# Performance work log

Hardware: AMD Instinct MI355X
Metric: run time of the kernel (lower is better)

## Reference

```python
import jax, jax.numpy as jnp
import numpy as np

N, D, DR, DA = 50000, 128, 64, 64
R, A = 2000, 5000
L, H = 2, 2
E, E2, EA = 400000, 800000, 400000


def setup_inputs() -> dict:
    key = jax.random.key(0)
    ks = jax.random.split(key, 8)
    rng = np.random.default_rng(0)

    ee = np.stack([rng.integers(0, N, E), rng.integers(0, N, E)], 1)
    ee = ee[np.lexsort((ee[:, 1], ee[:, 0]))]            # sorted unique-ish ent-ent edges
    seg_id = np.repeat(np.arange(E), 2)                  # 2 relation rows per edge
    er_rel = rng.integers(0, R, E2)
    er_index = np.stack([np.repeat(ee[:, 0], 2), er_rel], 1)   # (node, rel) pairs
    ea_index = np.stack([rng.integers(0, N, EA), rng.integers(0, A, EA)], 1)
    ea_index = ea_index[np.lexsort((ea_index[:, 1], ea_index[:, 0]))]

    s192 = 1.0 / np.sqrt(192.0)
    s320 = 1.0 / np.sqrt(320.0)
    return {
        "ent_emb": jax.random.normal(ks[0], (N, D), jnp.float32) * 0.1,
        "rel_emb": jax.random.normal(ks[1], (R, DR), jnp.float32) * 0.1,
        "attr_emb": jax.random.normal(ks[2], (A, DA), jnp.float32) * 0.1,
        "w_r": jax.random.normal(ks[3], (192, 1), jnp.float32) * s192,
        "b_r": jnp.zeros((1,), jnp.float32),
        "w_a": jax.random.normal(ks[4], (192, 1), jnp.float32) * s192,
        "b_a": jnp.zeros((1,), jnp.float32),
        "ent_attn_w": jax.random.normal(ks[5], (L, H, 192, 1), jnp.float32) * s192,
        "ent_attn_b": jnp.zeros((L, H, 1), jnp.float32),
        "con_attn_w": jax.random.normal(ks[6], (L, H, 320, 1), jnp.float32) * s320,
        "con_attn_b": jnp.zeros((L, H, 1), jnp.float32),
        "ee_index": jnp.asarray(ee, jnp.int32),
        "seg_id": jnp.asarray(seg_id, jnp.int32),
        "er_rel": jnp.asarray(er_rel, jnp.int32),
        "er_index": jnp.asarray(er_index, jnp.int32),
        "ea_index": jnp.asarray(ea_index, jnp.int32),
    }


def _leaky(v):
    return jnp.where(v > 0, v, 0.3 * v)  # LeakyReLU(alpha=0.3)


def _seg_softmax(vals, seg, n):
    m = jax.ops.segment_max(vals, seg, num_segments=n)
    e = jnp.exp(vals - m[seg])
    s = jax.ops.segment_sum(e, seg, num_segments=n)
    return e / s[seg]


def _forward(ent_emb, rel_emb, attr_emb, w_r, b_r, w_a, b_a,
             eaw, eab, caw, cab, ee_index, seg_id, er_rel, er_index, ea_index):
    n, d = ent_emb.shape
    nl, nh = eaw.shape[0], eaw.shape[1]
    dh = d // nh
    ne = ee_index.shape[0]

    def concept(idx, emb, w, b):
        feat = jnp.concatenate([ent_emb[idx[:, 0]], emb[idx[:, 1]]], axis=1)
        a = _leaky(feat @ w + b).reshape(-1)
        p = _seg_softmax(a, idx[:, 0], n)                      # tf.sparse.softmax per row
        return jax.nn.relu(jax.ops.segment_sum(p[:, None] * emb[idx[:, 1]], idx[:, 0], num_segments=n))

    concept_rel = concept(er_index, rel_emb, w_r, b_r)         # (N, DR)
    concept_attr = concept(ea_index, attr_emb, w_a, b_a)       # (N, DA)

    row, col = ee_index[:, 0], ee_index[:, 1]
    # softmax over all-ones sparse adj == neighbor mean
    deg = jax.ops.segment_sum(jnp.ones((ne,), ent_emb.dtype), row, num_segments=n)
    x = jax.ops.segment_sum(ent_emb[col], row, num_segments=n) / jnp.maximum(deg, 1.0)[:, None]

    # segment_mean of relation embeddings over duplicate (h,t) edges
    cnt = jax.ops.segment_sum(jnp.ones((er_rel.shape[0],), ent_emb.dtype), seg_id, num_segments=ne)
    rels_mean = jax.ops.segment_sum(rel_emb[er_rel], seg_id, num_segments=ne) / jnp.maximum(cnt, 1.0)[:, None]

    # concept features per edge (same for every layer/head -> hoisted)
    con_feat = jnp.concatenate([concept_rel[row], concept_attr[row], rels_mean,
                                concept_rel[col], concept_attr[col]], axis=1)  # (E, 320)

    layer_outs = []
    for l in range(nl):
        x = jax.nn.relu(x)
        heads = x.reshape(n, nh, dh)
        outs = []
        for h in range(nh):
            xe = heads[:, h, :]
            nf = xe[col]
            ef = jnp.concatenate([xe[row], rels_mean, nf], axis=1)      # (E, 192)
            ea = _leaky(ef @ eaw[l, h] + eab[l, h]).reshape(-1)
            ca = _leaky(con_feat @ caw[l, h] + cab[l, h]).reshape(-1)
            p = jax.nn.softmax(ea * ca)         # tf.nn.softmax over all edge values
            p = _seg_softmax(p, row, n)          # then tf.sparse.softmax per row
            outs.append(jax.ops.segment_sum(p[:, None] * nf, row, num_segments=n))
        x = jnp.tanh(jnp.concatenate(outs, axis=1))
        layer_outs.append(x)

    grat_out = jnp.concatenate(layer_outs, axis=1)                     # (N, L*D)
    ent_out = jnp.concatenate([grat_out, concept_rel, concept_attr], axis=1)
    conc = jnp.concatenate([concept_rel, concept_attr], axis=1)
    return ent_out, conc


def reference(ent_emb, rel_emb, attr_emb, w_r, b_r, w_a, b_a,
              ent_attn_w, ent_attn_b, con_attn_w, con_attn_b,
              ee_index, seg_id, er_rel, er_index, ea_index):
    return _forward(ent_emb, rel_emb, attr_emb, w_r, b_r, w_a, b_a,
                    ent_attn_w, ent_attn_b, con_attn_w, con_attn_b,
                    ee_index, seg_id, er_rel, er_index, ea_index)
```

## Files before the change

### kernel.cpp

```cpp
#include <hip/hip_runtime.h>
#include <math.h>

#define NENT 50000
#define RREL 2000
#define AATT 5000
#define EE   400000
#define E2   800000
#define EAE  400000
#define PB   2048

__device__ __forceinline__ float leaky(float v){ return v > 0.f ? v : 0.3f * v; }

__device__ __forceinline__ float wave_sum(float v){
#pragma unroll
  for (int m = 32; m; m >>= 1) v += __shfl_xor(v, m);
  return v;
}
__device__ __forceinline__ float sum16(float v){
#pragma unroll
  for (int m = 1; m < 16; m <<= 1) v += __shfl_xor(v, m);
  return v;
}

__device__ int lowb(const int* a, int n, int key){
  int lo = 0, hi = n;
  while (lo < hi){ int mid = (lo + hi) >> 1; if (a[2 * mid] < key) lo = mid + 1; else hi = mid; }
  return lo;
}

__global__ void k_ptr(const int* ee, const int* er, const int* ea,
                      int* pee, int* per, int* pea){
  int i = blockIdx.x * blockDim.x + threadIdx.x;
  if (i > NENT) return;
  pee[i] = lowb(ee, EE, i);
  per[i] = lowb(er, E2, i);
  pea[i] = lowb(ea, EAE, i);
}

__global__ void k_small(const float* rel_emb, const float* attr_emb,
                        const float* w_r, const float* w_a,
                        const float* eaw, const float* caw,
                        float* h_rel, float* h_attr, float4* HH0, float4* HH1){
  int t = blockIdx.x * blockDim.x + threadIdx.x;
  if (t < RREL){
    const float* e = rel_emb + (size_t)t * 64;
    float s = 0.f;
    for (int k = 0; k < 64; ++k) s += e[k] * w_r[128 + k];
    h_rel[t] = s;
    float hr[4], hc[4];
    for (int lh = 0; lh < 4; ++lh){
      float a = 0.f, c = 0.f;
      for (int k = 0; k < 64; ++k){
        a += e[k] * eaw[lh * 192 + 64 + k];
        c += e[k] * caw[lh * 320 + 128 + k];
      }
      hr[lh] = a; hc[lh] = c;
    }
    HH0[t] = make_float4(hr[0], hr[1], hc[0], hc[1]);
    HH1[t] = make_float4(hr[2], hr[3], hc[2], hc[3]);
  }
  if (t < AATT){
    const float* e = attr_emb + (size_t)t * 64;
    float s = 0.f;
    for (int k = 0; k < 64; ++k) s += e[k] * w_a[128 + k];
    h_attr[t] = s;
  }
}

__global__ void k_ent_tab(const float* ent_emb, const float* w_r, const float* w_a,
                          float* her, float* hea){
  int w = (blockIdx.x * blockDim.x + threadIdx.x) >> 6;
  int lane = threadIdx.x & 63;
  if (w >= NENT) return;
  float2 v = ((const float2*)(ent_emb + (size_t)w * 128))[lane];
  float2 a = ((const float2*)w_r)[lane];
  float2 b = ((const float2*)w_a)[lane];
  float sr = wave_sum(v.x * a.x + v.y * a.y);
  float sa = wave_sum(v.x * b.x + v.y * b.y);
  if (lane == 0){ her[w] = sr; hea[w] = sa; }
}

__global__ void k_cw(const int* er_idx, const int* ea_idx,
                     const float* her, const float* hea,
                     const float* h_rel, const float* h_attr,
                     const float* b_r, const float* b_a,
                     float* wr, float* wa){
  int e = blockIdx.x * blockDim.x + threadIdx.x;
  if (e < E2){
    int2 rc = ((const int2*)er_idx)[e];
    wr[e] = __expf(leaky(her[rc.x] + h_rel[rc.y] + b_r[0]));
  }
  if (e < EAE){
    int2 rc = ((const int2*)ea_idx)[e];
    wa[e] = __expf(leaky(hea[rc.x] + h_attr[rc.y] + b_a[0]));
  }
}

__device__ float4 concept_g(const float* wq, const int* idx, int beg, int end,
                            const float* emb, int p){
  float t = 0.f;
  for (int e = beg + p; e < end; e += 16) t += wq[e];
  t = sum16(t);
  float invz = (t > 0.f) ? (1.f / t) : 0.f;
  float4 acc = {0.f, 0.f, 0.f, 0.f};
  for (int c0 = beg; c0 < end; c0 += 8){
    int cnt = end - c0; if (cnt > 8) cnt = 8;
#pragma unroll
    for (int j = 0; j < 8; ++j){
      int e = c0 + ((j < cnt) ? j : 0);
      float wgt = wq[e] * invz;
      if (j >= cnt) wgt = 0.f;
      int obj = ((const int2*)idx)[e].y;
      float4 f = ((const float4*)(emb + (size_t)obj * 64))[p];
      acc.x = fmaf(wgt, f.x, acc.x); acc.y = fmaf(wgt, f.y, acc.y);
      acc.z = fmaf(wgt, f.z, acc.z); acc.w = fmaf(wgt, f.w, acc.w);
    }
  }
  acc.x = fmaxf(acc.x, 0.f); acc.y = fmaxf(acc.y, 0.f);
  acc.z = fmaxf(acc.z, 0.f); acc.w = fmaxf(acc.w, 0.f);
  return acc;
}

__global__ void k_phase1(const float* ent_emb, const float* rel_emb, const float* attr_emb,
                         const float* eaw, const float* caw,
                         const int* er_idx, const int* ea_idx, const int* ee,
                         const int* per, const int* pea, const int* pee,
                         const float* wr, const float* wa,
                         float4* UA0, float4* VB0, float4* UA1, float4* VB1,
                         float* out){
  int tid = blockIdx.x * blockDim.x + threadIdx.x;
  int lane = threadIdx.x & 63;
  int p = lane & 15;
  int w = (tid >> 6) * 4 + (lane >> 4);
  if (w >= NENT) return;
  float4 accR = concept_g(wr, er_idx, per[w], per[w + 1], rel_emb, p);
  float4 accA = concept_g(wa, ea_idx, pea[w], pea[w + 1], attr_emb, p);
  ((float4*)(out + (size_t)w * 384 + 256))[p] = accR;
  ((float4*)(out + (size_t)w * 384 + 320))[p] = accA;
  ((float4*)(out + (size_t)NENT * 384 + (size_t)w * 128))[p] = accR;
  ((float4*)(out + (size_t)NENT * 384 + (size_t)w * 128 + 64))[p] = accA;
  int beg = pee[w], end = pee[w + 1];
  float4 mx = {0.f,0.f,0.f,0.f}, my = {0.f,0.f,0.f,0.f};
  for (int c0 = beg; c0 < end; c0 += 4){
    int cnt = end - c0; if (cnt > 4) cnt = 4;
#pragma unroll
    for (int j = 0; j < 4; ++j){
      int e = c0 + ((j < cnt) ? j : 0);
      float msk = (j < cnt) ? 1.f : 0.f;
      int ce = ((const int2*)ee)[e].y;
      const float4* r = (const float4*)(ent_emb + (size_t)ce * 128);
      float4 q0 = r[p], q1 = r[p + 16];
      mx.x = fmaf(msk, q0.x, mx.x); mx.y = fmaf(msk, q0.y, mx.y);
      mx.z = fmaf(msk, q0.z, mx.z); mx.w = fmaf(msk, q0.w, mx.w);
      my.x = fmaf(msk, q1.x, my.x); my.y = fmaf(msk, q1.y, my.y);
      my.z = fmaf(msk, q1.z, my.z); my.w = fmaf(msk, q1.w, my.w);
    }
  }
  float invd = 1.f / fmaxf((float)(end - beg), 1.f);
  mx.x *= invd; mx.y *= invd; mx.z *= invd; mx.w *= invd;
  my.x *= invd; my.y *= invd; my.z *= invd; my.w *= invd;
  ((float4*)(out + (size_t)w * 384 + 128))[p] = mx;
  ((float4*)(out + (size_t)w * 384 + 192))[p] = my;
#pragma unroll
  for (int lh = 0; lh < 4; ++lh){
    const float* cw = caw + lh * 320;
    float4 c0 = *(const float4*)(cw + 4 * p);
    float4 c1 = *(const float4*)(cw + 64 + 4 * p);
    float4 c2 = *(const float4*)(cw + 192 + 4 * p);
    float4 c3 = *(const float4*)(cw + 256 + 4 * p);
    float av = accR.x*c0.x + accR.y*c0.y + accR.z*c0.z + accR.w*c0.w
             + accA.x*c1.x + accA.y*c1.y + accA.z*c1.z + accA.w*c1.w;
    float bv = accR.x*c2.x + accR.y*c2.y + accR.z*c2.z + accR.w*c2.w
             + accA.x*c3.x + accA.y*c3.y + accA.z*c3.z + accA.w*c3.w;
    av = sum16(av); bv = sum16(bv);
    if (p == 0){
      float4* U = (lh < 2) ? UA0 : UA1;
      float4* V = (lh < 2) ? VB0 : VB1;
      ((float*)(U + w))[2 + (lh & 1)] = av;
      ((float*)(V + w))[2 + (lh & 1)] = bv;
    }
  }
  {
    float e0 = fmaxf(mx.x,0.f), e1 = fmaxf(mx.y,0.f), e2 = fmaxf(mx.z,0.f), e3 = fmaxf(mx.w,0.f);
    float e4 = fmaxf(my.x,0.f), e5 = fmaxf(my.y,0.f), e6 = fmaxf(my.z,0.f), e7 = fmaxf(my.w,0.f);
    float4 u0 = *(const float4*)(eaw + 4 * p);
    float4 v0 = *(const float4*)(eaw + 128 + 4 * p);
    float4 u1 = *(const float4*)(eaw + 192 + 4 * p);
    float4 v1 = *(const float4*)(eaw + 192 + 128 + 4 * p);
    float pu0 = sum16(e0*u0.x + e1*u0.y + e2*u0.z + e3*u0.w);
    float pv0 = sum16(e0*v0.x + e1*v0.y + e2*v0.z + e3*v0.w);
    float pu1 = sum16(e4*u1.x + e5*u1.y + e6*u1.z + e7*u1.w);
    float pv1 = sum16(e4*v1.x + e5*v1.y + e6*v1.z + e7*v1.w);
    if (p == 0){
      ((float*)(UA0 + w))[0] = pu0; ((float*)(UA0 + w))[1] = pu1;
      ((float*)(VB0 + w))[0] = pv0; ((float*)(VB0 + w))[1] = pv1;
    }
  }
}

__global__ void k_se(const int* ee, const int* err,
                     const float4* UA, const float4* VB, const float4* HH,
                     const float* eab_l, const float* cab_l,
                     float2* s01, float* partials){
  int e = blockIdx.x * blockDim.x + threadIdx.x;
  int tid = threadIdx.x;
  __shared__ float sm0[4], sm1[4];
  float ex0 = 0.f, ex1 = 0.f;
  if (e < EE){
    int2 rc = ((const int2*)ee)[e];
    int2 rr = ((const int2*)err)[e];
    float4 ua = UA[rc.x], vb = VB[rc.y], h1 = HH[rr.x], h2 = HH[rr.y];
    float ea0 = ua.x + 0.5f * (h1.x + h2.x) + vb.x + eab_l[0];
    float ca0 = ua.z + 0.5f * (h1.z + h2.z) + vb.z + cab_l[0];
    ex0 = __expf(leaky(ea0) * leaky(ca0));
    float ea1 = ua.y + 0.5f * (h1.y + h2.y) + vb.y + eab_l[1];
    float ca1 = ua.w + 0.5f * (h1.w + h2.w) + vb.w + cab_l[1];
    ex1 = __expf(leaky(ea1) * leaky(ca1));
    s01[e] = make_float2(ex0, ex1);
  }
  float b0 = wave_sum(ex0), b1 = wave_sum(ex1);
  if ((tid & 63) == 0){ sm0[tid >> 6] = b0; sm1[tid >> 6] = b1; }
  __syncthreads();
  if (tid == 0)  partials[blockIdx.x]      = sm0[0] + sm0[1] + sm0[2] + sm0[3];
  if (tid == 64) partials[PB + blockIdx.x] = sm1[0] + sm1[1] + sm1[2] + sm1[3];
}

__global__ void k_final(const float* partials, float* scal, int nb){
  __shared__ float sm[1024];
  int tid = threadIdx.x;
  for (int h = 0; h < 2; ++h){
    float v = 0.f;
    for (int i = tid; i < nb; i += 1024) v += partials[h * PB + i];
    sm[tid] = v; __syncthreads();
    for (int s = 512; s; s >>= 1){
      if (tid < s) sm[tid] += sm[tid + s];
      __syncthreads();
    }
    if (tid == 0) scal[h] = sm[0];
    __syncthreads();
  }
}

__global__ void k_agg(const int* ee, const int* ptr, const float2* q01,
                      const float* scal, const float* xsrc, float* outp, int ocol,
                      const float* eaw_next, float4* UAn, float4* VBn){
  int tid = blockIdx.x * blockDim.x + threadIdx.x;
  int lane = threadIdx.x & 63;
  int p = lane & 15;
  int w = (tid >> 6) * 4 + (lane >> 4);
  if (w >= NENT) return;
  int beg = ptr[w], end = ptr[w + 1];
  float invZ0 = 1.f / scal[0], invZ1 = 1.f / scal[1];
  float4 a0 = {0.f,0.f,0.f,0.f}, a1 = {0.f,0.f,0.f,0.f};
  float4 b0 = {0.f,0.f,0.f,0.f}, b1 = {0.f,0.f,0.f,0.f};
  float T0 = 0.f, T1 = 0.f;
  for (int c0 = beg; c0 < end; c0 += 8){
    int cnt = end - c0; if (cnt > 8) cnt = 8;
#pragma unroll
    for (int j = 0; j < 8; ++j){
      int e = c0 + ((j < cnt) ? j : 0);
      float2 q = q01[e];
      float msk = (j < cnt) ? 1.f : 0.f;
      float s0 = q.x * msk, s1 = q.y * msk;
      T0 += s0; T1 += s1;
      int cj = ((const int2*)ee)[e].y;
      const float4* r = (const float4*)(xsrc + (size_t)cj * 384);
      float4 f0 = r[p], f1 = r[p + 16];
      f0.x = fmaxf(f0.x, 0.f); f0.y = fmaxf(f0.y, 0.f);
      f0.z = fmaxf(f0.z, 0.f); f0.w = fmaxf(f0.w, 0.f);
      f1.x = fmaxf(f1.x, 0.f); f1.y = fmaxf(f1.y, 0.f);
      f1.z = fmaxf(f1.z, 0.f); f1.w = fmaxf(f1.w, 0.f);
      b0.x = fmaf(msk, f0.x, b0.x); b0.y = fmaf(msk, f0.y, b0.y);
      b0.z = fmaf(msk, f0.z, b0.z); b0.w = fmaf(msk, f0.w, b0.w);
      b1.x = fmaf(msk, f1.x, b1.x); b1.y = fmaf(msk, f1.y, b1.y);
      b1.z = fmaf(msk, f1.z, b1.z); b1.w = fmaf(msk, f1.w, b1.w);
      a0.x = fmaf(s0, f0.x, a0.x); a0.y = fmaf(s0, f0.y, a0.y);
      a0.z = fmaf(s0, f0.z, a0.z); a0.w = fmaf(s0, f0.w, a0.w);
      a1.x = fmaf(s1, f1.x, a1.x); a1.y = fmaf(s1, f1.y, a1.y);
      a1.z = fmaf(s1, f1.z, a1.z); a1.w = fmaf(s1, f1.w, a1.w);
    }
  }
  float cnt = (float)(end - beg);
  float inv0 = (end > beg) ? (1.f / (cnt + invZ0 * T0)) : 0.f;
  float inv1 = (end > beg) ? (1.f / (cnt + invZ1 * T1)) : 0.f;
  float4 o0, o1;
  o0.x = tanhf((b0.x + invZ0 * a0.x) * inv0); o0.y = tanhf((b0.y + invZ0 * a0.y) * inv0);
  o0.z = tanhf((b0.z + invZ0 * a0.z) * inv0); o0.w = tanhf((b0.w + invZ0 * a0.w) * inv0);
  o1.x = tanhf((b1.x + invZ1 * a1.x) * inv1); o1.y = tanhf((b1.y + invZ1 * a1.y) * inv1);
  o1.z = tanhf((b1.z + invZ1 * a1.z) * inv1); o1.w = tanhf((b1.w + invZ1 * a1.w) * inv1);
  ((float4*)(outp + (size_t)w * 384 + ocol))[p]      = o0;
  ((float4*)(outp + (size_t)w * 384 + ocol + 64))[p] = o1;
  if (eaw_next){
    float e0 = fmaxf(o0.x,0.f), e1 = fmaxf(o0.y,0.f), e2 = fmaxf(o0.z,0.f), e3 = fmaxf(o0.w,0.f);
    float e4 = fmaxf(o1.x,0.f), e5 = fmaxf(o1.y,0.f), e6 = fmaxf(o1.z,0.f), e7 = fmaxf(o1.w,0.f);
    float4 u0 = *(const float4*)(eaw_next + 4 * p);
    float4 v0 = *(const float4*)(eaw_next + 128 + 4 * p);
    float4 u1 = *(const float4*)(eaw_next + 192 + 4 * p);
    float4 v1 = *(const float4*)(eaw_next + 192 + 128 + 4 * p);
    float pu0 = sum16(e0*u0.x + e1*u0.y + e2*u0.z + e3*u0.w);
    float pv0 = sum16(e0*v0.x + e1*v0.y + e2*v0.z + e3*v0.w);
    float pu1 = sum16(e4*u1.x + e5*u1.y + e6*u1.z + e7*u1.w);
    float pv1 = sum16(e4*v1.x + e5*v1.y + e6*v1.z + e7*v1.w);
    if (p == 0){
      ((float*)(UAn + w))[0] = pu0; ((float*)(UAn + w))[1] = pu1;
      ((float*)(VBn + w))[0] = pv0; ((float*)(VBn + w))[1] = pv1;
    }
  }
}

extern "C" void kernel_launch(void* const* d_in, const int* in_sizes, int n_in,
                              void* d_out, int out_size, void* d_ws, size_t ws_size,
                              hipStream_t stream){
  const float* ent_emb  = (const float*)d_in[0];
  const float* rel_emb  = (const float*)d_in[1];
  const float* attr_emb = (const float*)d_in[2];
  const float* w_r      = (const float*)d_in[3];
  const float* b_r      = (const float*)d_in[4];
  const float* w_a      = (const float*)d_in[5];
  const float* b_a      = (const float*)d_in[6];
  const float* eaw      = (const float*)d_in[7];
  const float* eab      = (const float*)d_in[8];
  const float* caw      = (const float*)d_in[9];
  const float* cab      = (const float*)d_in[10];
  const int*   ee       = (const int*)d_in[11];
  const int*   er_rel2  = (const int*)d_in[13];
  const int*   er_idx   = (const int*)d_in[14];
  const int*   ea_idx   = (const int*)d_in[15];
  float* out = (float*)d_out;

  int* pee = (int*)d_ws;
  int* per = pee + (NENT + 1);
  int* pea = per + (NENT + 1);
  float*  fbase = (float*)d_ws + 150004;
  float4* UA0 = (float4*)fbase;
  float4* VB0 = UA0 + NENT;
  float4* UA1 = VB0 + NENT;
  float4* VB1 = UA1 + NENT;
  float4* HH0 = VB1 + NENT;
  float4* HH1 = HH0 + RREL;
  float* her     = (float*)(HH1 + RREL);
  float* hea     = her + NENT;
  float* h_rel   = hea + NENT;
  float* h_attr  = h_rel + RREL;
  float* partials= h_attr + AATT;
  float* scal    = partials + 2 * PB;
  float* wr      = scal + 4;
  float* wa      = wr + E2;
  float2* s01    = (float2*)wr;

  const int nb = (EE + 255) / 256;
  const int gq = (NENT + 15) / 16;
  const int gw = (NENT + 3) / 4;

  k_ptr<<<(NENT + 1 + 255) / 256, 256, 0, stream>>>(ee, er_idx, ea_idx, pee, per, pea);
  k_small<<<(AATT + 255) / 256, 256, 0, stream>>>(rel_emb, attr_emb, w_r, w_a, eaw, caw,
                                                  h_rel, h_attr, HH0, HH1);
  k_ent_tab<<<gw, 256, 0, stream>>>(ent_emb, w_r, w_a, her, hea);
  k_cw<<<(E2 + 255) / 256, 256, 0, stream>>>(er_idx, ea_idx, her, hea,
                                             h_rel, h_attr, b_r, b_a, wr, wa);
  k_phase1<<<gq, 256, 0, stream>>>(ent_emb, rel_emb, attr_emb, eaw, caw,
                                   er_idx, ea_idx, ee, per, pea, pee, wr, wa,
                                   UA0, VB0, UA1, VB1, out);
  k_se<<<nb, 256, 0, stream>>>(ee, er_rel2, UA0, VB0, HH0, eab, cab, s01, partials);
  k_final<<<1, 1024, 0, stream>>>(partials, scal, nb);
  k_agg<<<gq, 256, 0, stream>>>(ee, pee, s01, scal, out + 128, out, 0,
                                eaw + 2 * 192, UA1, VB1);
  k_se<<<nb, 256, 0, stream>>>(ee, er_rel2, UA1, VB1, HH1, eab + 2, cab + 2, s01, partials);
  k_final<<<1, 1024, 0, stream>>>(partials, scal, nb);
  k_agg<<<gq, 256, 0, stream>>>(ee, pee, s01, scal, out, out, 128,
                                (const float*)nullptr, (float4*)nullptr, (float4*)nullptr);
}
```

Baseline: 216.5 us.

## Fuse preprocessing kernels, compute concept weights inline, fold final reduction into k_se

Merges the pointer, small-table and entity-table kernels into one block-partitioned launch. Drops the k_cw kernel and its edge-weight arrays: concept attention weights are recomputed inside phase1 and cached in shared memory for the first 64 edges per entity. The separate single-block final reduction is replaced by a last-block-done atomic counter inside k_se. Together these cut kernel launches and global traffic for the intermediate weight arrays. The cost is extra exp work in phase1, shared memory that may lower occupancy, and reliance on a threadfence/atomic pattern for correctness.

```diff
diff --git a/kernel.cpp b/kernel.cpp
--- a/kernel.cpp
+++ b/kernel.cpp
@@ -8,6 +8,8 @@
 #define E2   800000
 #define EAE  400000
 #define PB   2048
+#define PRE_PTR_B   196
+#define PRE_SMALL_B 20
 
 __device__ __forceinline__ float leaky(float v){ return v > 0.f ? v : 0.3f * v; }
 
@@ -28,89 +30,86 @@
   return lo;
 }
 
-__global__ void k_ptr(const int* ee, const int* er, const int* ea,
-                      int* pee, int* per, int* pea){
-  int i = blockIdx.x * blockDim.x + threadIdx.x;
-  if (i > NENT) return;
-  pee[i] = lowb(ee, EE, i);
-  per[i] = lowb(er, E2, i);
-  pea[i] = lowb(ea, EAE, i);
-}
-
-__global__ void k_small(const float* rel_emb, const float* attr_emb,
-                        const float* w_r, const float* w_a,
-                        const float* eaw, const float* caw,
-                        float* h_rel, float* h_attr, float4* HH0, float4* HH1){
-  int t = blockIdx.x * blockDim.x + threadIdx.x;
-  if (t < RREL){
-    const float* e = rel_emb + (size_t)t * 64;
-    float s = 0.f;
-    for (int k = 0; k < 64; ++k) s += e[k] * w_r[128 + k];
-    h_rel[t] = s;
-    float hr[4], hc[4];
-    for (int lh = 0; lh < 4; ++lh){
-      float a = 0.f, c = 0.f;
-      for (int k = 0; k < 64; ++k){
-        a += e[k] * eaw[lh * 192 + 64 + k];
-        c += e[k] * caw[lh * 320 + 128 + k];
+__global__ void k_pre(const int* ee, const int* er, const int* ea,
+                      int* pee, int* per, int* pea,
+                      const float* rel_emb, const float* attr_emb,
+                      const float* w_r, const float* w_a,
+                      const float* eaw, const float* caw,
+                      float* h_rel, float* h_attr, float4* HH0, float4* HH1,
+                      const float* ent_emb, float* her, float* hea, int* done){
+  int b = blockIdx.x;
+  if (b == 0 && threadIdx.x == 0){ done[0] = 0; done[1] = 0; }
+  if (b < PRE_PTR_B){
+    int i = b * 256 + threadIdx.x;
+    if (i <= NENT){
+      pee[i] = lowb(ee, EE, i);
+      per[i] = lowb(er, E2, i);
+      pea[i] = lowb(ea, EAE, i);
+    }
+  } else if (b < PRE_PTR_B + PRE_SMALL_B){
+    int t = (b - PRE_PTR_B) * 256 + threadIdx.x;
+    if (t < RREL){
+      const float* e = rel_emb + (size_t)t * 64;
+      float s = 0.f;
+      for (int k = 0; k < 64; ++k) s += e[k] * w_r[128 + k];
+      h_rel[t] = s;
+      float hr[4], hc[4];
+      for (int lh = 0; lh < 4; ++lh){
+        float a = 0.f, c = 0.f;
+        for (int k = 0; k < 64; ++k){
+          a += e[k] * eaw[lh * 192 + 64 + k];
+          c += e[k] * caw[lh * 320 + 128 + k];
+        }
+        hr[lh] = a; hc[lh] = c;
       }
-      hr[lh] = a; hc[lh] = c;
-    }
-    HH0[t] = make_float4(hr[0], hr[1], hc[0], hc[1]);
-    HH1[t] = make_float4(hr[2], hr[3], hc[2], hc[3]);
-  }
-  if (t < AATT){
-    const float* e = attr_emb + (size_t)t * 64;
-    float s = 0.f;
-    for (int k = 0; k < 64; ++k) s += e[k] * w_a[128 + k];
-    h_attr[t] = s;
-  }
-}
-
-__global__ void k_ent_tab(const float* ent_emb, const float* w_r, const float* w_a,
-                          float* her, float* hea){
-  int w = (blockIdx.x * blockDim.x + threadIdx.x) >> 6;
-  int lane = threadIdx.x & 63;
-  if (w >= NENT) return;
-  float2 v = ((const float2*)(ent_emb + (size_t)w * 128))[lane];
-  float2 a = ((const float2*)w_r)[lane];
-  float2 b = ((const float2*)w_a)[lane];
-  float sr = wave_sum(v.x * a.x + v.y * a.y);
-  float sa = wave_sum(v.x * b.x + v.y * b.y);
-  if (lane == 0){ her[w] = sr; hea[w] = sa; }
-}
-
-__global__ void k_cw(const int* er_idx, const int* ea_idx,
-                     const float* her, const float* hea,
-                     const float* h_rel, const float* h_attr,
-                     const float* b_r, const float* b_a,
-                     float* wr, float* wa){
-  int e = blockIdx.x * blockDim.x + threadIdx.x;
-  if (e < E2){
-    int2 rc = ((const int2*)er_idx)[e];
-    wr[e] = __expf(leaky(her[rc.x] + h_rel[rc.y] + b_r[0]));
-  }
-  if (e < EAE){
-    int2 rc = ((const int2*)ea_idx)[e];
-    wa[e] = __expf(leaky(hea[rc.x] + h_attr[rc.y] + b_a[0]));
-  }
-}
-
-__device__ float4 concept_g(const float* wq, const int* idx, int beg, int end,
-                            const float* emb, int p){
+      HH0[t] = make_float4(hr[0], hr[1], hc[0], hc[1]);
+      HH1[t] = make_float4(hr[2], hr[3], hc[2], hc[3]);
+    }
+    if (t < AATT){
+      const float* e = attr_emb + (size_t)t * 64;
+      float s = 0.f;
+      for (int k = 0; k < 64; ++k) s += e[k] * w_a[128 + k];
+      h_attr[t] = s;
+    }
+  } else {
+    int w = (((b - PRE_PTR_B - PRE_SMALL_B) * 256 + (int)threadIdx.x) >> 6);
+    int lane = threadIdx.x & 63;
+    if (w >= NENT) return;
+    float2 v = ((const float2*)(ent_emb + (size_t)w * 128))[lane];
+    float2 a = ((const float2*)w_r)[lane];
+    float2 bb = ((const float2*)w_a)[lane];
+    float sr = wave_sum(v.x * a.x + v.y * a.y);
+    float sa = wave_sum(v.x * bb.x + v.y * bb.y);
+    if (lane == 0){ her[w] = sr; hea[w] = sa; }
+  }
+}
+
+__device__ float4 concept_g(float he, const float* h_tab, const int* idx,
+                            int beg, int end, const float* emb, int p,
+                            float* swq, int* sobj){
+  int len = end - beg;
   float t = 0.f;
-  for (int e = beg + p; e < end; e += 16) t += wq[e];
+  for (int k = p; k < len; k += 16){
+    int obj = ((const int2*)idx)[beg + k].y;
+    float wq = __expf(leaky(he + h_tab[obj]));
+    if (k < 64){ swq[k] = wq; sobj[k] = obj; }
+    t += wq;
+  }
   t = sum16(t);
   float invz = (t > 0.f) ? (1.f / t) : 0.f;
   float4 acc = {0.f, 0.f, 0.f, 0.f};
-  for (int c0 = beg; c0 < end; c0 += 8){
-    int cnt = end - c0; if (cnt > 8) cnt = 8;
+  for (int c0 = 0; c0 < len; c0 += 8){
+    int cnt = len - c0; if (cnt > 8) cnt = 8;
 #pragma unroll
     for (int j = 0; j < 8; ++j){
-      int e = c0 + ((j < cnt) ? j : 0);
-      float wgt = wq[e] * invz;
-      if (j >= cnt) wgt = 0.f;
-      int obj = ((const int2*)idx)[e].y;
+      int k = c0 + ((j < cnt) ? j : 0);
+      int obj; float wq;
+      if (k < 64){ obj = sobj[k]; wq = swq[k]; }
+      else {
+        obj = ((const int2*)idx)[beg + k].y;
+        wq = __expf(leaky(he + h_tab[obj]));
+      }
+      float wgt = (j < cnt) ? wq * invz : 0.f;
       float4 f = ((const float4*)(emb + (size_t)obj * 64))[p];
       acc.x = fmaf(wgt, f.x, acc.x); acc.y = fmaf(wgt, f.y, acc.y);
       acc.z = fmaf(wgt, f.z, acc.z); acc.w = fmaf(wgt, f.w, acc.w);
@@ -125,16 +124,23 @@
                          const float* eaw, const float* caw,
                          const int* er_idx, const int* ea_idx, const int* ee,
                          const int* per, const int* pea, const int* pee,
-                         const float* wr, const float* wa,
+                         const float* her, const float* hea,
+                         const float* h_rel, const float* h_attr,
+                         const float* b_r, const float* b_a,
                          float4* UA0, float4* VB0, float4* UA1, float4* VB1,
                          float* out){
+  __shared__ float swq[16][64];
+  __shared__ int   sobj[16][64];
   int tid = blockIdx.x * blockDim.x + threadIdx.x;
   int lane = threadIdx.x & 63;
   int p = lane & 15;
+  int g = threadIdx.x >> 4;
   int w = (tid >> 6) * 4 + (lane >> 4);
   if (w >= NENT) return;
-  float4 accR = concept_g(wr, er_idx, per[w], per[w + 1], rel_emb, p);
-  float4 accA = concept_g(wa, ea_idx, pea[w], pea[w + 1], attr_emb, p);
+  float heR = her[w] + b_r[0];
+  float heA = hea[w] + b_a[0];
+  float4 accR = concept_g(heR, h_rel, er_idx, per[w], per[w + 1], rel_emb, p, swq[g], sobj[g]);
+  float4 accA = concept_g(heA, h_attr, ea_idx, pea[w], pea[w + 1], attr_emb, p, swq[g], sobj[g]);
   ((float4*)(out + (size_t)w * 384 + 256))[p] = accR;
   ((float4*)(out + (size_t)w * 384 + 320))[p] = accA;
   ((float4*)(out + (size_t)NENT * 384 + (size_t)w * 128))[p] = accR;
@@ -201,10 +207,11 @@
 __global__ void k_se(const int* ee, const int* err,
                      const float4* UA, const float4* VB, const float4* HH,
                      const float* eab_l, const float* cab_l,
-                     float2* s01, float* partials){
+                     float2* s01, float* partials, float* scal, int* done, int nb){
   int e = blockIdx.x * blockDim.x + threadIdx.x;
   int tid = threadIdx.x;
   __shared__ float sm0[4], sm1[4];
+  __shared__ int lastf;
   float ex0 = 0.f, ex1 = 0.f;
   if (e < EE){
     int2 rc = ((const int2*)ee)[e];
@@ -221,23 +228,24 @@
   float b0 = wave_sum(ex0), b1 = wave_sum(ex1);
   if ((tid & 63) == 0){ sm0[tid >> 6] = b0; sm1[tid >> 6] = b1; }
   __syncthreads();
-  if (tid == 0)  partials[blockIdx.x]      = sm0[0] + sm0[1] + sm0[2] + sm0[3];
-  if (tid == 64) partials[PB + blockIdx.x] = sm1[0] + sm1[1] + sm1[2] + sm1[3];
-}
-
-__global__ void k_final(const float* partials, float* scal, int nb){
-  __shared__ float sm[1024];
-  int tid = threadIdx.x;
-  for (int h = 0; h < 2; ++h){
-    float v = 0.f;
-    for (int i = tid; i < nb; i += 1024) v += partials[h * PB + i];
-    sm[tid] = v; __syncthreads();
-    for (int s = 512; s; s >>= 1){
-      if (tid < s) sm[tid] += sm[tid + s];
+  if (tid == 0){
+    partials[blockIdx.x]      = sm0[0] + sm0[1] + sm0[2] + sm0[3];
+    partials[PB + blockIdx.x] = sm1[0] + sm1[1] + sm1[2] + sm1[3];
+    __threadfence();
+    lastf = (atomicAdd(done, 1) == nb - 1) ? 1 : 0;
+  }
+  __syncthreads();
+  if (lastf){
+    __threadfence();
+    float v0 = 0.f, v1 = 0.f;
+    for (int i = tid; i < nb; i += 256){ v0 += partials[i]; v1 += partials[PB + i]; }
+    __shared__ float r0[256], r1[256];
+    r0[tid] = v0; r1[tid] = v1; __syncthreads();
+    for (int s = 128; s; s >>= 1){
+      if (tid < s){ r0[tid] += r0[tid + s]; r1[tid] += r1[tid + s]; }
       __syncthreads();
     }
-    if (tid == 0) scal[h] = sm[0];
-    __syncthreads();
+    if (tid == 0){ scal[0] = r0[0]; scal[1] = r1[0]; }
   }
 }
 
@@ -344,29 +352,27 @@
   float* h_attr  = h_rel + RREL;
   float* partials= h_attr + AATT;
   float* scal    = partials + 2 * PB;
-  float* wr      = scal + 4;
-  float* wa      = wr + E2;
-  float2* s01    = (float2*)wr;
+  int*   done    = (int*)(scal + 4);
+  float2* s01    = (float2*)(done + 4);
 
   const int nb = (EE + 255) / 256;
   const int gq = (NENT + 15) / 16;
-  const int gw = (NENT + 3) / 4;
-
-  k_ptr<<<(NENT + 1 + 255) / 256, 256, 0, stream>>>(ee, er_idx, ea_idx, pee, per, pea);
-  k_small<<<(AATT + 255) / 256, 256, 0, stream>>>(rel_emb, attr_emb, w_r, w_a, eaw, caw,
-                                                  h_rel, h_attr, HH0, HH1);
-  k_ent_tab<<<gw, 256, 0, stream>>>(ent_emb, w_r, w_a, her, hea);
-  k_cw<<<(E2 + 255) / 256, 256, 0, stream>>>(er_idx, ea_idx, her, hea,
-                                             h_rel, h_attr, b_r, b_a, wr, wa);
+  const int npre = PRE_PTR_B + PRE_SMALL_B + (NENT * 64 + 255) / 256;
+
+  k_pre<<<npre, 256, 0, stream>>>(ee, er_idx, ea_idx, pee, per, pea,
+                                  rel_emb, attr_emb, w_r, w_a, eaw, caw,
+                                  h_rel, h_attr, HH0, HH1,
+                                  ent_emb, her, hea, done);
   k_phase1<<<gq, 256, 0, stream>>>(ent_emb, rel_emb, attr_emb, eaw, caw,
-                                   er_idx, ea_idx, ee, per, pea, pee, wr, wa,
+                                   er_idx, ea_idx, ee, per, pea, pee,
+                                   her, hea, h_rel, h_attr, b_r, b_a,
                                    UA0, VB0, UA1, VB1, out);
-  k_se<<<nb, 256, 0, stream>>>(ee, er_rel2, UA0, VB0, HH0, eab, cab, s01, partials);
-  k_final<<<1, 1024, 0, stream>>>(partials, scal, nb);
+  k_se<<<nb, 256, 0, stream>>>(ee, er_rel2, UA0, VB0, HH0, eab, cab,
+                               s01, partials, scal, done + 0, nb);
   k_agg<<<gq, 256, 0, stream>>>(ee, pee, s01, scal, out + 128, out, 0,
                                 eaw + 2 * 192, UA1, VB1);
-  k_se<<<nb, 256, 0, stream>>>(ee, er_rel2, UA1, VB1, HH1, eab + 2, cab + 2, s01, partials);
-  k_final<<<1, 1024, 0, stream>>>(partials, scal, nb);
+  k_se<<<nb, 256, 0, stream>>>(ee, er_rel2, UA1, VB1, HH1, eab + 2, cab + 2,
+                               s01, partials, scal, done + 1, nb);
   k_agg<<<gq, 256, 0, stream>>>(ee, pee, s01, scal, out, out, 128,
                                 (const float*)nullptr, (float4*)nullptr, (float4*)nullptr);
 }
```

Result: slower. 265.7 us (+22.7%).
